# Kernel tuning notes

Hardware: AMD Instinct MI355X
Metric: run time of the kernel (lower is better)

## Reference

```python
import jax, jax.numpy as jnp
import numpy as np
from jax import lax

DILATIONS = (1, 3, 9, 27, 81, 1)
C = 128        # model channels
UP = 2048      # up-projection channels
K = 512        # filterbank kernel size
NZ = 64        # non_zero_elements kept by sparsify
B = 2
N = 32768      # n_samples


def conv1d(x, w, b, dilation=1, padding='VALID'):
    # x: [B,Cin,T], w: [Cout,Cin,Kw]
    y = lax.conv_general_dilated(x, w, (1,), padding, rhs_dilation=(dilation,),
                                 dimension_numbers=('NCH', 'OIH', 'NCH'))
    return y if b is None else y + b[None, :, None]


def dilated_stack(x, ws, bs, causal_past):
    # residual stack of kernel-2 dilated causal convs; 'only-past' pads left, 'only-future' pads right
    for i, d in enumerate(DILATIONS):
        pad = ((0, 0), (0, 0), (d, 0)) if causal_past else ((0, 0), (0, 0), (0, d))
        h = conv1d(jnp.pad(x, pad), ws[i], bs[i], dilation=d)
        x = x + jax.nn.leaky_relu(h, 0.2)
    return x


def sparsify_topk(x, k):
    # keep top-k values (soft=True: keep magnitudes) over flattened (C,T) per sample
    b = x.shape[0]
    flat = x.reshape(b, -1)
    vals, idx = lax.top_k(flat, k)
    out = jnp.zeros_like(flat).at[jnp.arange(b)[:, None], idx].set(vals)
    return out.reshape(x.shape)


def setup_inputs() -> dict:
    key = jax.random.key(0)
    ks = jax.random.split(key, 11)
    s = 0.1  # weight_init
    return {
        'x': jax.random.normal(ks[0], (B, 1, N), jnp.float32),
        'fb': jax.random.normal(ks[1], (C, 1, K), jnp.float32) * s,        # filterbank
        'enc_w': jax.random.normal(ks[2], (6, C, C, 2), jnp.float32) * s,
        'enc_b': jnp.zeros((6, C), jnp.float32),
        'up_w': jax.random.normal(ks[3], (UP, C, 1), jnp.float32) * s,
        'up_b': jnp.zeros((UP,), jnp.float32),
        'down_w': jax.random.normal(ks[4], (C, UP, 1), jnp.float32) * s,
        'down_b': jnp.zeros((C,), jnp.float32),
        'dec_w': jax.random.normal(ks[5], (6, C, C, 2), jnp.float32) * s,
        'dec_b': jnp.zeros((6, C), jnp.float32),
    }


def reference(x, fb, enc_w, enc_b, up_w, up_b, down_w, down_b, dec_w, dec_b):
    # filterbank analysis: [B,1,N] -> [B,C,N]
    spec = conv1d(x, fb, None, 1, ((K // 2, K // 2 - 1),))
    enc = dilated_stack(spec, enc_w, enc_b, causal_past=False)  # 'only-future'
    enc = conv1d(enc, up_w, up_b)            # [B,2048,N]
    enc = sparsify_topk(enc, NZ)             # 64 nonzeros per sample
    enc = conv1d(enc, down_w, down_b)        # [B,128,N]
    dec = dilated_stack(enc, dec_w, dec_b, causal_past=True)    # 'only-past'
    dec = jnp.pad(dec, ((0, 0), (0, 0), (0, 1)))                # F.pad(decoded, (0,1))
    # transposed convolve back to waveform: flipped filterbank, sum over channels
    kt = jnp.flip(fb, -1).transpose(1, 0, 2)  # [1,C,K]
    final = conv1d(dec, kt, None, 1, ((K // 2 - 1, K // 2),))[:, :, :N]
    return final
```

## Files before the change

### kernel.cpp

```cpp
#include <hip/hip_runtime.h>
#include <stdint.h>

#define NB  2
#define NC  128
#define NT  32768
#define KFB 512
#define NUP 2048
#define CAP 14336

typedef unsigned int u32;
typedef unsigned short u16;
typedef short s16;
typedef float f32x4 __attribute__((ext_vector_type(4)));
typedef s16 short8 __attribute__((ext_vector_type(8)));
typedef u32 u32x4 __attribute__((ext_vector_type(4)));

__device__ __forceinline__ u32 f2key(float v){
  u32 u = __float_as_uint(v);
  return (u & 0x80000000u) ? ~u : (u | 0x80000000u);
}
__device__ __forceinline__ float key2f(u32 k){
  u32 u = (k & 0x80000000u) ? (k & 0x7FFFFFFFu) : ~k;
  return __uint_as_float(u);
}
__device__ __forceinline__ u16 bf16rn(float v){
  u32 u = __float_as_uint(v);
  return (u16)((u + 0x7FFFu + ((u>>16)&1u)) >> 16);
}
__device__ __forceinline__ u32 packhl(float v){
  u16 h = bf16rn(v);
  u16 lo = bf16rn(v - __uint_as_float(((u32)h)<<16));
  return ((u32)h<<16) | lo;
}
__device__ __forceinline__ void unpack8(const u32* p, short8& xh, short8& xl){
  u32x4 r0 = *(const u32x4*)p;
  u32x4 r1 = *(const u32x4*)(p + 4);
  union { u32 u[4]; short8 v; } H, L;
  H.u[0] = __builtin_amdgcn_perm(r0.y, r0.x, 0x07060302u);
  H.u[1] = __builtin_amdgcn_perm(r0.w, r0.z, 0x07060302u);
  H.u[2] = __builtin_amdgcn_perm(r1.y, r1.x, 0x07060302u);
  H.u[3] = __builtin_amdgcn_perm(r1.w, r1.z, 0x07060302u);
  L.u[0] = __builtin_amdgcn_perm(r0.y, r0.x, 0x05040100u);
  L.u[1] = __builtin_amdgcn_perm(r0.w, r0.z, 0x05040100u);
  L.u[2] = __builtin_amdgcn_perm(r1.y, r1.x, 0x05040100u);
  L.u[3] = __builtin_amdgcn_perm(r1.w, r1.z, 0x05040100u);
  xh = H.v; xl = L.v;
}

#define RS 132

__global__ __launch_bounds__(256) void k_prep(const float* __restrict__ encw,
    const float* __restrict__ decw, const float* __restrict__ upw,
    const float* __restrict__ fbw,
    u16* __restrict__ wdil, u16* __restrict__ wup, u16* __restrict__ wfb,
    u32* __restrict__ h1, u32* __restrict__ h2, int* __restrict__ counts){
  int g = blockIdx.x*256 + threadIdx.x;
  if (g < 2048) h1[g] = 0u;
  else if (g < 4096) h2[g-2048] = 0u;
  if (g < NB) counts[g] = 0;
  if (g < 49152){
    int l = g & 63, mt = (g>>6)&7, s = (g>>9)&7, layer = g>>12;
    const float* W = (layer < 6) ? (encw + (size_t)layer*NC*NC*2)
                                 : (decw + (size_t)(layer-6)*NC*NC*2);
    int co = mt*16 + (l & 15);
    int kb = s*32 + ((l>>4)<<3);
    union { u16 h[8]; u32x4 q; } H, L;
    #pragma unroll
    for (int j=0;j<8;++j){
      int k = kb + j;
      float v = W[((size_t)co*NC + (k&127))*2 + (k>>7)];
      u16 h = bf16rn(v);
      H.h[j] = h;
      L.h[j] = bf16rn(v - __uint_as_float(((u32)h)<<16));
    }
    int unit = g >> 6;
    *(u32x4*)(wdil + (size_t)unit*1024 + (l<<3)) = H.q;
    *(u32x4*)(wdil + (size_t)unit*1024 + 512 + (l<<3)) = L.q;
  } else if (g < 81920){
    int g2 = g - 49152;
    int l = g2 & 63, umt = (g2>>6)&127, s = g2>>13;
    int u = umt*16 + (l & 15);
    int kb = s*32 + ((l>>4)<<3);
    union { u16 h[8]; u32x4 q; } H, L;
    #pragma unroll
    for (int j=0;j<8;++j){
      float v = upw[(size_t)u*NC + kb + j];
      u16 h = bf16rn(v);
      H.h[j] = h;
      L.h[j] = bf16rn(v - __uint_as_float(((u32)h)<<16));
    }
    int unit = g2 >> 6;
    *(u32x4*)(wup + (size_t)unit*1024 + (l<<3)) = H.q;
    *(u32x4*)(wup + (size_t)unit*1024 + 512 + (l<<3)) = L.q;
  } else if (g < 90112){
    int g3 = g - 81920;
    int l = g3 & 63, mt = (g3>>6)&7, s = g3>>9;
    int c = mt*16 + (l & 15);
    int kb = s*32 + ((l>>4)<<3);
    union { u16 h[8]; u32x4 q; } H, L;
    #pragma unroll
    for (int j=0;j<8;++j){
      float v = fbw[(size_t)c*KFB + kb + j];
      u16 h = bf16rn(v);
      H.h[j] = h;
      L.h[j] = bf16rn(v - __uint_as_float(((u32)h)<<16));
    }
    int unit = g3 >> 6;
    *(u32x4*)(wfb + (size_t)unit*1024 + (l<<3)) = H.q;
    *(u32x4*)(wfb + (size_t)unit*1024 + 512 + (l<<3)) = L.q;
  }
}

__global__ __launch_bounds__(256) void k_fb(const float* __restrict__ x,
    const u16* __restrict__ wfb, float* __restrict__ spec){
  __shared__ u32 xw[640];
  const int tid = threadIdx.x;
  const int t0 = blockIdx.x << 7;
  const int b  = blockIdx.y;
  const int lane = tid & 63, w = tid >> 6;
  const int wy = w >> 1, wx = w & 1;
  const int quad = lane >> 4, l15 = lane & 15;
  for (int i = tid; i < 640; i += 256){
    int t = t0 - 256 + i;
    float v = ((u32)t < (u32)NT) ? x[b*NT + t] : 0.0f;
    xw[i] = packhl(v);
  }
  __syncthreads();
  f32x4 acc[4][4] = {};
  for (int s = 0; s < 16; ++s){
    short8 ah[4], al[4];
    #pragma unroll
    for (int mt=0; mt<4; ++mt){
      const u16* p = wfb + (size_t)(s*8 + wy*4 + mt)*1024 + (lane<<3);
      ah[mt] = *(const short8*)p;
      al[mt] = *(const short8*)(p + 512);
    }
    short8 xh[4], xl[4];
    #pragma unroll
    for (int nt=0; nt<4; ++nt){
      int base = s*32 + quad*8 + (wx<<6) + (nt<<4) + l15;
      u32 r[8];
      #pragma unroll
      for (int j=0;j<8;++j) r[j] = xw[base + j];
      union { u32 u[4]; short8 v; } H, L;
      H.u[0] = __builtin_amdgcn_perm(r[1], r[0], 0x07060302u);
      H.u[1] = __builtin_amdgcn_perm(r[3], r[2], 0x07060302u);
      H.u[2] = __builtin_amdgcn_perm(r[5], r[4], 0x07060302u);
      H.u[3] = __builtin_amdgcn_perm(r[7], r[6], 0x07060302u);
      L.u[0] = __builtin_amdgcn_perm(r[1], r[0], 0x05040100u);
      L.u[1] = __builtin_amdgcn_perm(r[3], r[2], 0x05040100u);
      L.u[2] = __builtin_amdgcn_perm(r[5], r[4], 0x05040100u);
      L.u[3] = __builtin_amdgcn_perm(r[7], r[6], 0x05040100u);
      xh[nt] = H.v; xl[nt] = L.v;
    }
    #pragma unroll
    for (int mt=0; mt<4; ++mt){
      #pragma unroll
      for (int nt=0; nt<4; ++nt){
        acc[mt][nt] = __builtin_amdgcn_mfma_f32_16x16x32_bf16(ah[mt], xh[nt], acc[mt][nt], 0,0,0);
        acc[mt][nt] = __builtin_amdgcn_mfma_f32_16x16x32_bf16(ah[mt], xl[nt], acc[mt][nt], 0,0,0);
        acc[mt][nt] = __builtin_amdgcn_mfma_f32_16x16x32_bf16(al[mt], xh[nt], acc[mt][nt], 0,0,0);
      }
    }
  }
  #pragma unroll
  for (int mt=0; mt<4; ++mt){
    #pragma unroll
    for (int r=0; r<4; ++r){
      const int c = (wy<<6) + (mt<<4) + (quad<<2) + r;
      float* po = spec + (size_t)(b*NC+c)*NT + t0 + (wx<<6) + l15;
      #pragma unroll
      for (int nt=0; nt<4; ++nt) po[nt<<4] = acc[mt][nt][r];
    }
  }
}

__global__ __launch_bounds__(1024,4) void k_stack(const float* __restrict__ xin,
    float* __restrict__ xout, const u16* __restrict__ wf,
    const float* __restrict__ biases, int mode){
  extern __shared__ u32 lx[];
  const int tid = threadIdx.x;
  const int b  = blockIdx.y;
  const int T0 = blockIdx.x << 7;
  const int row0g = mode ? (T0 - 122) : T0;
  const int lane = tid & 63, w = tid >> 6;
  const int wm = w >> 2, wn = w & 3;
  const int quad = lane >> 4, l15 = lane & 15;
  {
    const float* xb = xin + (size_t)b*NC*NT;
    const int row = tid & 255;
    const int ci0 = (tid >> 8) << 5;
    const int tg = row0g + row;
    const bool ok = ((u32)tg < (u32)NT);
    const float* src = xb + (size_t)ci0*NT + tg;
    u32* dst = lx + row*RS + ci0;
    #pragma unroll
    for (int g=0; g<8; ++g){
      u32x4 q;
      #pragma unroll
      for (int k=0;k<4;++k){
        float v = ok ? src[(size_t)(g*4 + k)*NT] : 0.0f;
        q[k] = packhl(v);
      }
      *(u32x4*)(dst + g*4) = q;
    }
  }
  const int dils[6] = {1,3,9,27,81,1};
  const int Hrem[6] = {121,118,109,82,1,0};
  #pragma unroll 1
  for (int l = 0; l < 6; ++l){
    const int d = dils[l];
    const int o0 = mode ? -d : 0;
    const int o1 = mode ? 0 : d;
    const int lo = mode ? (122 - Hrem[l]) : 0;
    const int hi = mode ? 250 : (128 + Hrem[l]);
    const u16* wl = wf + ((size_t)l << 16);
    __syncthreads();
    bool act[4];
    #pragma unroll
    for (int nt=0;nt<4;++nt){
      const int Tst = (wn<<6) + (nt<<4);
      act[nt] = (Tst + 16 > lo) && (Tst < hi);
    }
    f32x4 acc[2][4] = {};
    short8 cah[2], cal[2], nah[2], nal[2];
    {
      const u16* p0 = wl + (size_t)(((wm<<1) + 0) << 10) + (lane<<3);
      const u16* p1 = wl + (size_t)(((wm<<1) + 1) << 10) + (lane<<3);
      cah[0] = *(const short8*)p0; cal[0] = *(const short8*)(p0 + 512);
      cah[1] = *(const short8*)p1; cal[1] = *(const short8*)(p1 + 512);
    }
    #pragma unroll 1
    for (int s = 0; s < 8; ++s){
      const int sn = (s < 7) ? (s + 1) : 7;
      const u16* p0 = wl + (size_t)(((sn<<3) + (wm<<1) + 0) << 10) + (lane<<3);
      const u16* p1 = wl + (size_t)(((sn<<3) + (wm<<1) + 1) << 10) + (lane<<3);
      nah[0] = *(const short8*)p0; nal[0] = *(const short8*)(p0 + 512);
      nah[1] = *(const short8*)p1; nal[1] = *(const short8*)(p1 + 512);
      const int o = (s >= 4) ? o1 : o0;
      const int cig = (s & 3) << 5;
      #pragma unroll
      for (int nt=0;nt<4;++nt){
        if (!act[nt]) continue;
        const int T = ((wn<<6) + (nt<<4) + l15 + o) & 255;
        const int idx = T*RS + cig + (quad<<3);
        short8 xh, xl;
        unpack8(&lx[idx], xh, xl);
        acc[0][nt] = __builtin_amdgcn_mfma_f32_16x16x32_bf16(cah[0], xh, acc[0][nt], 0,0,0);
        acc[0][nt] = __builtin_amdgcn_mfma_f32_16x16x32_bf16(cah[0], xl, acc[0][nt], 0,0,0);
        acc[0][nt] = __builtin_amdgcn_mfma_f32_16x16x32_bf16(cal[0], xh, acc[0][nt], 0,0,0);
        acc[1][nt] = __builtin_amdgcn_mfma_f32_16x16x32_bf16(cah[1], xh, acc[1][nt], 0,0,0);
        acc[1][nt] = __builtin_amdgcn_mfma_f32_16x16x32_bf16(cah[1], xl, acc[1][nt], 0,0,0);
        acc[1][nt] = __builtin_amdgcn_mfma_f32_16x16x32_bf16(cal[1], xh, acc[1][nt], 0,0,0);
      }
      cah[0] = nah[0]; cal[0] = nal[0];
      cah[1] = nah[1]; cal[1] = nal[1];
    }
    __syncthreads();
    const float* bl = biases + l*NC;
    const bool last = (l == 5);
    #pragma unroll
    for (int mt=0;mt<2;++mt){
      const int cobase = (wm<<5) + (mt<<4) + (quad<<2);
      float bv[4];
      #pragma unroll
      for (int r=0;r<4;++r) bv[r] = bl[cobase + r];
      #pragma unroll
      for (int nt=0;nt<4;++nt){
        if (!act[nt]) continue;
        const int T = (wn<<6) + (nt<<4) + l15;
        const int idx = T*RS + cobase;
        u32x4 xo = *(const u32x4*)&lx[idx];
        const int tg = row0g + T;
        const bool tvld = ((u32)tg < (u32)NT);
        float nv[4];
        #pragma unroll
        for (int r=0;r<4;++r){
          float oldv = __uint_as_float(xo[r] & 0xFFFF0000u) + __uint_as_float(xo[r] << 16);
          float h = acc[mt][nt][r] + bv[r];
          h = (h >= 0.f) ? h : 0.2f*h;
          float xn = oldv + h;
          nv[r] = tvld ? xn : 0.0f;
        }
        if (!last){
          u32x4 np;
          #pragma unroll
          for (int r=0;r<4;++r) np[r] = packhl(nv[r]);
          *(u32x4*)&lx[idx] = np;
        } else {
          const bool rowok = mode ? (T >= 122 && T < 250) : (T < 128);
          if (rowok){
            float* po = xout + (size_t)(b*NC + cobase)*NT + tg;
            #pragma unroll
            for (int r=0;r<4;++r) po[(size_t)r*NT] = nv[r];
          }
        }
      }
    }
  }
}

__global__ __launch_bounds__(256) void k_sub(const float* __restrict__ enc,
                                             const float* __restrict__ upw,
                                             const float* __restrict__ upb,
                                             u32* __restrict__ keys,
                                             u32* __restrict__ hist1){
  const int u0 = blockIdx.x * 64;
  const int i0 = blockIdx.y * 256;
  const int b  = blockIdx.z;
  __shared__ float uwl[32][68];
  __shared__ float ec[32][260];
  __shared__ u32 lh[1024];
  const int tid = threadIdx.x;
  for (int i=tid;i<1024;i+=256) lh[i] = 0u;
  const int ug = tid & 15;
  const int ig = tid >> 4;
  float acc[4][16];
  #pragma unroll
  for (int i=0;i<4;++i){
    #pragma unroll
    for (int j=0;j<16;++j) acc[i][j]=0.0f;
  }
  for (int c0=0;c0<NC;c0+=32){
    __syncthreads();
    #pragma unroll
    for (int i=0;i<8;++i){
      int flat = i*256+tid;
      uwl[flat & 31][flat >> 5] = upw[(size_t)(u0 + (flat>>5))*NC + c0 + (flat&31)];
    }
    #pragma unroll
    for (int i=0;i<32;++i){
      int flat = i*256+tid;
      ec[flat >> 8][flat & 255] = enc[(size_t)(b*NC + c0 + (flat>>8))*NT + (size_t)(i0 + (flat&255))*32];
    }
    __syncthreads();
    #pragma unroll 2
    for (int cc=0;cc<32;++cc){
      float a[4], bb[16];
      *(float4*)&a[0] = *(const float4*)&uwl[cc][ug*4];
      #pragma unroll
      for (int m=0;m<4;++m)
        *(float4*)&bb[m*4] = *(const float4*)&ec[cc][ig*16 + m*4];
      #pragma unroll
      for (int i=0;i<4;++i){
        #pragma unroll
        for (int j=0;j<16;++j)
          acc[i][j] = fmaf(a[i], bb[j], acc[i][j]);
      }
    }
  }
  #pragma unroll
  for (int i=0;i<4;++i){
    int u = u0 + ug*4 + i;
    float ub = upb[u];
    #pragma unroll
    for (int j=0;j<16;++j){
      float v = acc[i][j] + ub;
      u32 k = f2key(v);
      keys[(size_t)(b*NUP + u)*1024 + i0 + ig*16 + j] = k;
      atomicAdd(&lh[k >> 22], 1u);
    }
  }
  __syncthreads();
  for (int i=tid;i<1024;i+=256){
    u32 c = lh[i];
    if (c) atomicAdd(&hist1[b*1024 + i], c);
  }
}

__global__ __launch_bounds__(256) void k_sel(const u32* __restrict__ hist,
                                             u32* __restrict__ cstar,
                                             u32* __restrict__ nab,
                                             u32* __restrict__ t0key,
                                             int phase){
  const int b = blockIdx.x;
  __shared__ u32 s1[1024];
  __shared__ u32 s2[1024];
  __shared__ int red[256];
  const int tid = threadIdx.x;
  for (int i=tid;i<1024;i+=256) s1[i] = hist[b*1024 + i];
  __syncthreads();
  u32* cur = s1; u32* nxt = s2;
  for (int off=1; off<1024; off<<=1){
    for (int i=tid;i<1024;i+=256){
      u32 v = cur[i];
      if (i + off < 1024) v += cur[i+off];
      nxt[i] = v;
    }
    __syncthreads();
    u32* t = cur; cur = nxt; nxt = t;
  }
  u32 off0 = (phase==1) ? 0u : nab[b];
  int best = -1;
  for (int i=tid;i<1024;i+=256)
    if (off0 + cur[i] >= 64u && i > best) best = i;
  red[tid] = best;
  __syncthreads();
  for (int st=128; st>0; st>>=1){
    if (tid < st) red[tid] = max(red[tid], red[tid+st]);
    __syncthreads();
  }
  if (tid == 0){
    int bi = (red[0] < 0) ? 0 : red[0];
    if (phase == 1){
      cstar[b] = (u32)bi;
      nab[b] = (bi < 1023) ? cur[bi+1] : 0u;
    } else {
      t0key[b] = (cstar[b] << 22) | (((u32)bi) << 12);
    }
  }
}

__global__ void k_h2(const u32* __restrict__ keys, const u32* __restrict__ cstar,
                     u32* __restrict__ hist2){
  const u32 c0 = cstar[0], c1 = cstar[1];
  int i = blockIdx.x*256 + threadIdx.x;
  const int total = NB*NUP*1024;
  const int stride = gridDim.x*256;
  for (; i < total; i += stride){
    u32 k = keys[i];
    u32 cs = (i >> 21) ? c1 : c0;
    if ((k >> 22) == cs) atomicAdd(&hist2[((u32)(i>>21)<<10) + ((k>>12) & 1023u)], 1u);
  }
}

#define RSH 136
__global__ __launch_bounds__(256,2) void k_up(const float* __restrict__ enc,
    const u16* __restrict__ wf, const float* __restrict__ upb,
    const u32* __restrict__ t0key, float* __restrict__ cval,
    int* __restrict__ cidx, int* __restrict__ counts){
  extern __shared__ u16 ls[];
  u16* lhh = ls;
  u16* lll = ls + 128*RSH;
  const int tid = threadIdx.x;
  const int t0 = blockIdx.x << 7;
  const int b  = blockIdx.y;
  const int lane = tid & 63, w = tid >> 6;
  const int wy = w >> 1, wx = w & 1;
  const int quad = lane >> 4, l15 = lane & 15;
  {
    const float* xb = enc + (size_t)b*NC*NT + t0;
    const int row = tid >> 1;
    const int ci0 = (tid & 1) << 6;
    const float* src = xb + (size_t)ci0*NT + row;
    u16* dh = lhh + row*RSH + ci0;
    u16* dl = lll + row*RSH + ci0;
    #pragma unroll
    for (int g=0; g<8; ++g){
      union { u16 h[8]; short8 v; } H, L;
      #pragma unroll
      for (int j=0;j<8;++j){
        float v = src[(size_t)(g*8 + j)*NT];
        u16 hh = bf16rn(v);
        H.h[j] = hh;
        L.h[j] = bf16rn(v - __uint_as_float(((u32)hh)<<16));
      }
      *(short8*)(dh + (g<<3)) = H.v;
      *(short8*)(dl + (g<<3)) = L.v;
    }
  }
  __syncthreads();
  float T0 = key2f(t0key[b]);
  T0 -= fabsf(T0)*3e-4f + 1e-5f;
  short8 cah[4], cal[4], nah[4], nal[4];
  {
    #pragma unroll
    for (int mt=0;mt<4;++mt){
      const u16* p = wf + (size_t)((wy*4 + mt) << 10) + (lane<<3);
      cah[mt] = *(const short8*)p; cal[mt] = *(const short8*)(p + 512);
    }
  }
  f32x4 acc[4][4] = {};
  #pragma unroll 1
  for (int ss = 0; ss < 64; ++ss){
    const int uc = ss >> 2, s = ss & 3;
    const int ssn = (ss < 63) ? (ss + 1) : 63;
    const int ucn = ssn >> 2, sn = ssn & 3;
    #pragma unroll
    for (int mt=0;mt<4;++mt){
      const u16* p = wf + (size_t)((sn*128 + ucn*8 + wy*4 + mt) << 10) + (lane<<3);
      nah[mt] = *(const short8*)p; nal[mt] = *(const short8*)(p + 512);
    }
    const int cig = s << 5;
    #pragma unroll
    for (int nt=0;nt<4;++nt){
      const int T = (wx<<6) + (nt<<4) + l15;
      const int base = T*RSH + cig + (quad<<3);
      short8 xh = *(const short8*)&lhh[base];
      short8 xl = *(const short8*)&lll[base];
      #pragma unroll
      for (int mt=0;mt<4;++mt){
        acc[mt][nt] = __builtin_amdgcn_mfma_f32_16x16x32_bf16(cah[mt], xh, acc[mt][nt], 0,0,0);
        acc[mt][nt] = __builtin_amdgcn_mfma_f32_16x16x32_bf16(cah[mt], xl, acc[mt][nt], 0,0,0);
        acc[mt][nt] = __builtin_amdgcn_mfma_f32_16x16x32_bf16(cal[mt], xh, acc[mt][nt], 0,0,0);
      }
    }
    if (s == 3){
      #pragma unroll
      for (int mt=0; mt<4; ++mt){
        #pragma unroll
        for (int r=0; r<4; ++r){
          int u = uc*128 + (wy<<6) + (mt<<4) + (quad<<2) + r;
          float ub = upb[u];
          #pragma unroll
          for (int nt=0; nt<4; ++nt){
            float v = acc[mt][nt][r] + ub;
            if (v >= T0){
              int slot = atomicAdd(&counts[b], 1);
              if (slot < CAP){
                cval[b*CAP + slot] = v;
                cidx[b*CAP + slot] = u*NT + (t0 + (wx<<6) + (nt<<4) + l15);
              }
            }
          }
        }
      }
      #pragma unroll
      for (int mt=0;mt<4;++mt)
        #pragma unroll
        for (int nt=0;nt<4;++nt) acc[mt][nt] = (f32x4){0.f,0.f,0.f,0.f};
    }
    #pragma unroll
    for (int mt=0;mt<4;++mt){ cah[mt] = nah[mt]; cal[mt] = nal[mt]; }
  }
}

__global__ __launch_bounds__(256) void k_top(const float* __restrict__ cval,
                                             const int* __restrict__ cidx,
                                             const int* __restrict__ counts,
                                             float* __restrict__ tv,
                                             int* __restrict__ ti){
  const int b = blockIdx.x;
  __shared__ float lv[CAP];
  __shared__ float sv[256];
  __shared__ int   si[256];
  const int tid = threadIdx.x;
  int n = counts[b]; if (n > CAP) n = CAP;
  if (n <= 8192){
    float v[32];
    #pragma unroll
    for (int r=0;r<32;++r){
      int i = r*256 + tid;
      v[r] = (i < n) ? cval[b*CAP+i] : -3.4e38f;
    }
    const int lane = tid & 63, wv = tid >> 6;
    for (int r=0;r<64;++r){
      float best = v[0]; int bidx = 0;
      #pragma unroll
      for (int k=1;k<32;++k){ if (v[k] > best){ best = v[k]; bidx = k; } }
      int gi = bidx*256 + tid;
      #pragma unroll
      for (int off=32; off>0; off>>=1){
        float ov = __shfl_down(best, off);
        int oi = __shfl_down(gi, off);
        if (ov > best){ best = ov; gi = oi; }
      }
      if (lane == 0){ sv[wv] = best; si[wv] = gi; }
      __syncthreads();
      if (tid == 0){
        float bb = sv[0]; int bbi = si[0];
        #pragma unroll
        for (int k=1;k<4;++k) if (sv[k] > bb){ bb = sv[k]; bbi = si[k]; }
        si[4] = bbi;
        if (bb > -3.0e38f){ tv[b*64+r] = bb; ti[b*64+r] = cidx[b*CAP + bbi]; }
        else { tv[b*64+r] = 0.0f; ti[b*64+r] = 0; }
      }
      __syncthreads();
      int wini = si[4];
      if ((wini & 255) == tid) v[wini >> 8] = -3.4e38f;
    }
  } else {
    for (int i=tid;i<n;i+=256) lv[i] = cval[b*CAP+i];
    __syncthreads();
    for (int r=0;r<64;++r){
      float best = -3.4e38f; int bi = -1;
      for (int i=tid;i<n;i+=256){
        float v = lv[i];
        if (v > best){ best = v; bi = i; }
      }
      sv[tid]=best; si[tid]=bi;
      __syncthreads();
      for (int st=128; st>0; st>>=1){
        if (tid < st && sv[tid+st] > sv[tid]){ sv[tid]=sv[tid+st]; si[tid]=si[tid+st]; }
        __syncthreads();
      }
      if (tid == 0){
        int kb = si[0];
        if (kb >= 0){
          tv[b*64+r] = sv[0];
          ti[b*64+r] = cidx[b*CAP+kb];
          lv[kb] = -3.4e38f;
        } else { tv[b*64+r] = 0.0f; ti[b*64+r] = 0; }
      }
      __syncthreads();
    }
  }
}

__global__ void k_dec0(float* __restrict__ dst, const float* __restrict__ dnb,
                       const float* __restrict__ dnw,
                       const float* __restrict__ tv, const int* __restrict__ ti){
  const int b = blockIdx.x >> 7, c = blockIdx.x & 127;
  float v = dnb[c];
  float4 vv; vv.x=v; vv.y=v; vv.z=v; vv.w=v;
  float* row = dst + (size_t)(b*NC+c)*NT;
  for (int i=threadIdx.x; i < NT/4; i += 256) *(float4*)&row[i*4] = vv;
  __syncthreads();
  if (threadIdx.x < 64){
    int r = threadIdx.x;
    float sv = tv[b*64+r];
    int idx = ti[b*64+r];
    int u = idx / NT, t = idx - u*NT;
    atomicAdd(&row[t], dnw[(size_t)c*NUP + u] * sv);
  }
}

#define TS 8192
#define WR 545
__global__ __launch_bounds__(512) void k_syn(const float* __restrict__ dec,
                                             const float* __restrict__ fb,
                                             float* __restrict__ part){
  const int ts = blockIdx.x;
  const int c  = blockIdx.y;
  const int b  = blockIdx.z;
  const int t0 = ts * TS;
  __shared__ float win2[16*WR];
  __shared__ float fbl[512];
  const int tid = threadIdx.x;
  const int tl = tid * 16;
  float acc[16];
  #pragma unroll
  for (int j=0;j<16;++j) acc[j] = 0.0f;
  for (int i=tid; i < TS+511; i += 512){
    int t = t0 - 255 + i;
    win2[(i & 15)*WR + (i >> 4)] = ((u32)t < (u32)NT) ? dec[(size_t)(b*NC+c)*NT + t] : 0.0f;
  }
  if (tid < 512) fbl[tid] = fb[c*KFB + tid];
  __syncthreads();
  float w[23];
  #pragma unroll
  for (int k=0;k<23;++k){
    int i = tl + 504 + k;
    w[k] = win2[(i & 15)*WR + (i >> 4)];
  }
  for (int G=0; G<64; ++G){
    float4 f0 = *(const float4*)&fbl[G*8];
    float4 f1 = *(const float4*)&fbl[G*8+4];
    float fq[8] = {f0.x, f0.y, f0.z, f0.w, f1.x, f1.y, f1.z, f1.w};
    #pragma unroll
    for (int q=0;q<8;++q){
      #pragma unroll
      for (int jj=0;jj<16;++jj)
        acc[jj] = fmaf(fq[q], w[7-q+jj], acc[jj]);
    }
    if (G != 63){
      #pragma unroll
      for (int k=22;k>=8;--k) w[k] = w[k-8];
      #pragma unroll
      for (int k=0;k<8;++k){
        int i = tl + 496 - 8*G + k;
        w[k] = win2[(i & 15)*WR + (i >> 4)];
      }
    }
  }
  float* po = &part[(size_t)(c*NB + b)*NT + t0 + tl];
  #pragma unroll
  for (int m=0;m<4;++m){
    float4 ov; ov.x=acc[m*4+0]; ov.y=acc[m*4+1]; ov.z=acc[m*4+2]; ov.w=acc[m*4+3];
    *(float4*)&po[m*4] = ov;
  }
}

__global__ void k_red(const float* __restrict__ part, float* __restrict__ out){
  int i4 = blockIdx.x*256 + threadIdx.x;
  float4 s; s.x=0.f; s.y=0.f; s.z=0.f; s.w=0.f;
  #pragma unroll 4
  for (int c=0;c<128;++c){
    float4 p = *(const float4*)&part[(size_t)c*(NB*NT) + (size_t)i4*4];
    s.x += p.x; s.y += p.y; s.z += p.z; s.w += p.w;
  }
  *(float4*)&out[(size_t)i4*4] = s;
}

extern "C" void kernel_launch(void* const* d_in, const int* in_sizes, int n_in,
                              void* d_out, int out_size, void* d_ws, size_t ws_size,
                              hipStream_t stream){
  const float* x    = (const float*)d_in[0];
  const float* fb   = (const float*)d_in[1];
  const float* encw = (const float*)d_in[2];
  const float* encb = (const float*)d_in[3];
  const float* upw  = (const float*)d_in[4];
  const float* upb  = (const float*)d_in[5];
  const float* dnw  = (const float*)d_in[6];
  const float* dnb  = (const float*)d_in[7];
  const float* decw = (const float*)d_in[8];
  const float* decb = (const float*)d_in[9];
  float* out = (float*)d_out;
  char* ws = (char*)d_ws;

  size_t o = 0;
  float* bufA = (float*)(ws + o); o += (size_t)NB*NC*NT*4;
  float* bufB = (float*)(ws + o); o += (size_t)NB*NC*NT*4;
  u32*  keys  = (u32*)(ws + o);   o += (size_t)NB*NUP*1024*4;
  u32*  hist1 = (u32*)(ws + o);   o += 1024*NB*4;
  u32*  hist2 = (u32*)(ws + o);   o += 1024*NB*4;
  u32*  cstar = (u32*)(ws + o);   o += 64;
  u32*  nab   = (u32*)(ws + o);   o += 64;
  u32*  t0k   = (u32*)(ws + o);   o += 64;
  int*  cnt   = (int*)(ws + o);   o += 64;
  float* tv   = (float*)(ws + o); o += NB*64*4;
  int*  ti    = (int*)(ws + o);   o += NB*64*4;
  float* cval = (float*)(ws + o); o += (size_t)NB*CAP*4;
  int*  cidx  = (int*)(ws + o);   o += (size_t)NB*CAP*4;
  u16*  wdil  = (u16*)(ws + o);   o += (size_t)12*65536*2;
  u16*  wup   = (u16*)(ws + o);   o += (size_t)4*128*1024*2;
  u16*  wfb   = (u16*)(ws + o);   o += (size_t)128*1024*2;
  float* part = bufA;

  k_prep<<<dim3(352), dim3(256), 0, stream>>>(encw, decw, upw, fb, wdil, wup, wfb, hist1, hist2, cnt);
  k_fb<<<dim3(256,NB), dim3(256), 0, stream>>>(x, wfb, bufA);

  k_stack<<<dim3(256,NB), dim3(1024), 256*RS*4, stream>>>(bufA, bufB, wdil, encb, 0);

  k_sub<<<dim3(32,4,NB), dim3(256), 0, stream>>>(bufB, upw, upb, keys, hist1);
  k_sel<<<dim3(NB), dim3(256), 0, stream>>>(hist1, cstar, nab, t0k, 1);
  k_h2 <<<dim3(4096), dim3(256), 0, stream>>>(keys, cstar, hist2);
  k_sel<<<dim3(NB), dim3(256), 0, stream>>>(hist2, cstar, nab, t0k, 2);
  k_up <<<dim3(256,NB), dim3(256), 2*128*RSH*2, stream>>>(bufB, wup, upb, t0k, cval, cidx, cnt);
  k_top<<<dim3(NB), dim3(256), 0, stream>>>(cval, cidx, cnt, tv, ti);

  k_dec0<<<dim3(NB*NC), dim3(256), 0, stream>>>(bufA, dnb, dnw, tv, ti);

  k_stack<<<dim3(256,NB), dim3(1024), 256*RS*4, stream>>>(bufA, bufB, wdil + (size_t)6*65536, decb, 1);

  k_syn<<<dim3(4,128,NB), dim3(512), 0, stream>>>(bufB, fb, part);
  k_red<<<dim3(64), dim3(256), 0, stream>>>(part, out);
}
```

Baseline: 906.4 us.

## Use single-bf16 decoder dilated stack and retile synthesis kernel

Adds k_stack2 for the decoder residual stack. It keeps activations in shared memory as a single bf16 value instead of a hi/lo split pair, which halves LDS footprint and drops one MFMA per tile step (4 instead of 6). The weight prefetch double-buffer in k_stack is removed in favour of loading weights each step. The synthesis kernel moves to 4096-sample tiles with 256 threads to get more blocks. Dropping the low bf16 part loses precision in the decoder activations, which risks tolerance failures.

```diff
diff --git a/kernel.cpp b/kernel.cpp
--- a/kernel.cpp
+++ b/kernel.cpp
@@ -14,6 +14,7 @@
 typedef float f32x4 __attribute__((ext_vector_type(4)));
 typedef s16 short8 __attribute__((ext_vector_type(8)));
 typedef u32 u32x4 __attribute__((ext_vector_type(4)));
+typedef u32 u32x2 __attribute__((ext_vector_type(2)));
 
 __device__ __forceinline__ u32 f2key(float v){
   u32 u = __float_as_uint(v);
@@ -48,6 +49,7 @@
 }
 
 #define RS 132
+#define RSH 136
 
 __global__ __launch_bounds__(256) void k_prep(const float* __restrict__ encw,
     const float* __restrict__ decw, const float* __restrict__ upw,
@@ -223,20 +225,15 @@
       act[nt] = (Tst + 16 > lo) && (Tst < hi);
     }
     f32x4 acc[2][4] = {};
-    short8 cah[2], cal[2], nah[2], nal[2];
-    {
-      const u16* p0 = wl + (size_t)(((wm<<1) + 0) << 10) + (lane<<3);
-      const u16* p1 = wl + (size_t)(((wm<<1) + 1) << 10) + (lane<<3);
-      cah[0] = *(const short8*)p0; cal[0] = *(const short8*)(p0 + 512);
-      cah[1] = *(const short8*)p1; cal[1] = *(const short8*)(p1 + 512);
-    }
     #pragma unroll 1
     for (int s = 0; s < 8; ++s){
-      const int sn = (s < 7) ? (s + 1) : 7;
-      const u16* p0 = wl + (size_t)(((sn<<3) + (wm<<1) + 0) << 10) + (lane<<3);
-      const u16* p1 = wl + (size_t)(((sn<<3) + (wm<<1) + 1) << 10) + (lane<<3);
-      nah[0] = *(const short8*)p0; nal[0] = *(const short8*)(p0 + 512);
-      nah[1] = *(const short8*)p1; nal[1] = *(const short8*)(p1 + 512);
+      short8 cah[2], cal[2];
+      #pragma unroll
+      for (int mt=0;mt<2;++mt){
+        const u16* p = wl + (size_t)(((s<<3) + (wm<<1) + mt) << 10) + (lane<<3);
+        cah[mt] = *(const short8*)p;
+        cal[mt] = *(const short8*)(p + 512);
+      }
       const int o = (s >= 4) ? o1 : o0;
       const int cig = (s & 3) << 5;
       #pragma unroll
@@ -253,8 +250,6 @@
         acc[1][nt] = __builtin_amdgcn_mfma_f32_16x16x32_bf16(cah[1], xl, acc[1][nt], 0,0,0);
         acc[1][nt] = __builtin_amdgcn_mfma_f32_16x16x32_bf16(cal[1], xh, acc[1][nt], 0,0,0);
       }
-      cah[0] = nah[0]; cal[0] = nal[0];
-      cah[1] = nah[1]; cal[1] = nal[1];
     }
     __syncthreads();
     const float* bl = biases + l*NC;
@@ -300,6 +295,118 @@
   }
 }
 
+__global__ __launch_bounds__(1024,8) void k_stack2(const float* __restrict__ xin,
+    float* __restrict__ xout, const u16* __restrict__ wf,
+    const float* __restrict__ biases){
+  extern __shared__ u16 lx2[];
+  const int tid = threadIdx.x;
+  const int b  = blockIdx.y;
+  const int T0 = blockIdx.x << 7;
+  const int row0g = T0 - 122;
+  const int lane = tid & 63, w = tid >> 6;
+  const int wm = w >> 2, wn = w & 3;
+  const int quad = lane >> 4, l15 = lane & 15;
+  {
+    const float* xb = xin + (size_t)b*NC*NT;
+    const int row = tid & 255;
+    const int ci0 = (tid >> 8) << 5;
+    const int tg = row0g + row;
+    const bool ok = ((u32)tg < (u32)NT);
+    const float* src = xb + (size_t)ci0*NT + tg;
+    u16* dst = lx2 + row*RSH + ci0;
+    #pragma unroll
+    for (int g=0; g<4; ++g){
+      union { u16 h[8]; short8 v; } H;
+      #pragma unroll
+      for (int j=0;j<8;++j){
+        float v = ok ? src[(size_t)(g*8 + j)*NT] : 0.0f;
+        H.h[j] = bf16rn(v);
+      }
+      *(short8*)(dst + (g<<3)) = H.v;
+    }
+  }
+  const int dils[6] = {1,3,9,27,81,1};
+  const int Hrem[6] = {121,118,109,82,1,0};
+  #pragma unroll 1
+  for (int l = 0; l < 6; ++l){
+    const int d = dils[l];
+    const int o0 = -d, o1 = 0;
+    const int lo = 122 - Hrem[l];
+    const u16* wl = wf + ((size_t)l << 16);
+    __syncthreads();
+    bool act[4];
+    #pragma unroll
+    for (int nt=0;nt<4;++nt){
+      const int Tst = (wn<<6) + (nt<<4);
+      act[nt] = (Tst + 16 > lo);
+    }
+    f32x4 acc[2][4] = {};
+    #pragma unroll 1
+    for (int s = 0; s < 8; ++s){
+      short8 cah[2], cal[2];
+      #pragma unroll
+      for (int mt=0;mt<2;++mt){
+        const u16* p = wl + (size_t)(((s<<3) + (wm<<1) + mt) << 10) + (lane<<3);
+        cah[mt] = *(const short8*)p;
+        cal[mt] = *(const short8*)(p + 512);
+      }
+      const int o = (s >= 4) ? o1 : o0;
+      const int cig = (s & 3) << 5;
+      #pragma unroll
+      for (int nt=0;nt<4;++nt){
+        if (!act[nt]) continue;
+        const int T = ((wn<<6) + (nt<<4) + l15 + o) & 255;
+        const int base = T*RSH + cig + (quad<<3);
+        short8 xh = *(const short8*)&lx2[base];
+        acc[0][nt] = __builtin_amdgcn_mfma_f32_16x16x32_bf16(cah[0], xh, acc[0][nt], 0,0,0);
+        acc[0][nt] = __builtin_amdgcn_mfma_f32_16x16x32_bf16(cal[0], xh, acc[0][nt], 0,0,0);
+        acc[1][nt] = __builtin_amdgcn_mfma_f32_16x16x32_bf16(cah[1], xh, acc[1][nt], 0,0,0);
+        acc[1][nt] = __builtin_amdgcn_mfma_f32_16x16x32_bf16(cal[1], xh, acc[1][nt], 0,0,0);
+      }
+    }
+    __syncthreads();
+    const float* bl = biases + l*NC;
+    const bool last = (l == 5);
+    #pragma unroll
+    for (int mt=0;mt<2;++mt){
+      const int cobase = (wm<<5) + (mt<<4) + (quad<<2);
+      float bv[4];
+      #pragma unroll
+      for (int r=0;r<4;++r) bv[r] = bl[cobase + r];
+      #pragma unroll
+      for (int nt=0;nt<4;++nt){
+        if (!act[nt]) continue;
+        const int T = (wn<<6) + (nt<<4) + l15;
+        const int base = T*RSH + cobase;
+        union { u16 h[4]; u32x2 q; } HH;
+        HH.q = *(const u32x2*)&lx2[base];
+        const int tg = row0g + T;
+        const bool tvld = ((u32)tg < (u32)NT);
+        float nv[4];
+        #pragma unroll
+        for (int r=0;r<4;++r){
+          float oldv = __uint_as_float(((u32)HH.h[r])<<16);
+          float h = acc[mt][nt][r] + bv[r];
+          h = (h >= 0.f) ? h : 0.2f*h;
+          float xn = oldv + h;
+          nv[r] = tvld ? xn : 0.0f;
+        }
+        if (!last){
+          #pragma unroll
+          for (int r=0;r<4;++r) HH.h[r] = bf16rn(nv[r]);
+          *(u32x2*)&lx2[base] = HH.q;
+        } else {
+          if (T >= 122 && T < 250){
+            float* po = xout + (size_t)(b*NC + cobase)*NT + tg;
+            #pragma unroll
+            for (int r=0;r<4;++r) po[(size_t)r*NT] = nv[r];
+          }
+        }
+      }
+    }
+  }
+}
+
 __global__ __launch_bounds__(256) void k_sub(const float* __restrict__ enc,
                                              const float* __restrict__ upw,
                                              const float* __restrict__ upb,
@@ -424,7 +531,6 @@
   }
 }
 
-#define RSH 136
 __global__ __launch_bounds__(256,2) void k_up(const float* __restrict__ enc,
     const u16* __restrict__ wf, const float* __restrict__ upb,
     const u32* __restrict__ t0key, float* __restrict__ cval,
@@ -615,33 +721,32 @@
   }
 }
 
-#define TS 8192
-#define WR 545
-__global__ __launch_bounds__(512) void k_syn(const float* __restrict__ dec,
+#define TS 4096
+__global__ __launch_bounds__(256) void k_syn(const float* __restrict__ dec,
                                              const float* __restrict__ fb,
                                              float* __restrict__ part){
   const int ts = blockIdx.x;
   const int c  = blockIdx.y;
   const int b  = blockIdx.z;
   const int t0 = ts * TS;
-  __shared__ float win2[16*WR];
+  __shared__ float win2[16*289 + 8];
   __shared__ float fbl[512];
   const int tid = threadIdx.x;
   const int tl = tid * 16;
   float acc[16];
   #pragma unroll
   for (int j=0;j<16;++j) acc[j] = 0.0f;
-  for (int i=tid; i < TS+511; i += 512){
+  for (int i=tid; i < TS+511; i += 256){
     int t = t0 - 255 + i;
-    win2[(i & 15)*WR + (i >> 4)] = ((u32)t < (u32)NT) ? dec[(size_t)(b*NC+c)*NT + t] : 0.0f;
-  }
-  if (tid < 512) fbl[tid] = fb[c*KFB + tid];
+    win2[(i & 15)*289 + (i >> 4)] = ((u32)t < (u32)NT) ? dec[(size_t)(b*NC+c)*NT + t] : 0.0f;
+  }
+  for (int i=tid; i<512; i+=256) fbl[i] = fb[c*KFB + i];
   __syncthreads();
   float w[23];
   #pragma unroll
   for (int k=0;k<23;++k){
     int i = tl + 504 + k;
-    w[k] = win2[(i & 15)*WR + (i >> 4)];
+    w[k] = win2[(i & 15)*289 + (i >> 4)];
   }
   for (int G=0; G<64; ++G){
     float4 f0 = *(const float4*)&fbl[G*8];
@@ -659,7 +764,7 @@
       #pragma unroll
       for (int k=0;k<8;++k){
         int i = tl + 496 - 8*G + k;
-        w[k] = win2[(i & 15)*WR + (i >> 4)];
+        w[k] = win2[(i & 15)*289 + (i >> 4)];
       }
     }
   }
@@ -731,8 +836,8 @@
 
   k_dec0<<<dim3(NB*NC), dim3(256), 0, stream>>>(bufA, dnb, dnw, tv, ti);
 
-  k_stack<<<dim3(256,NB), dim3(1024), 256*RS*4, stream>>>(bufA, bufB, wdil + (size_t)6*65536, decb, 1);
-
-  k_syn<<<dim3(4,128,NB), dim3(512), 0, stream>>>(bufB, fb, part);
+  k_stack2<<<dim3(256,NB), dim3(1024), 256*RSH*2, stream>>>(bufA, bufB, wdil + (size_t)6*65536, decb);
+
+  k_syn<<<dim3(8,128,NB), dim3(256), 0, stream>>>(bufB, fb, part);
   k_red<<<dim3(64), dim3(256), 0, stream>>>(part, out);
 }
```

Measured after the change: 811.2 us. 10.5% less time.
